# Performance work log

Hardware: AMD Instinct MI355X
Metric: run time of the kernel (lower is better)

## Reference

```python
import jax, jax.numpy as jnp
import numpy as np

B, T, C = 2, 2048, 2048
NH, G, HS = 16, 4, 128          # heads, kv groups, head dim
QPK = NH // G                    # queries per kv group
K = 4                            # conv kernel width
WIN = 512                        # sliding window (local_window)
SCALE = 1.0 / np.sqrt(HS)


def causal_conv1d_silu(x, w):
    # x: [B, T, D] channels-last, w: [D, K] depthwise kernel; causal left-pad then SiLU
    xp = jnp.pad(x, ((0, 0), (K - 1, 0), (0, 0)))
    out = sum(w[None, None, :, k] * xp[:, k:k + T, :] for k in range(K))
    return jax.nn.silu(out)


def apply_rope(x, cos, sin):
    # x: [B, T, H, HS], cos/sin: [T, HS//2]; non-interleaved halves rotation
    d = cos.shape[-1]
    x1, x2 = x[..., :d], x[..., d:]
    c = cos[None, :, None, :]
    s = sin[None, :, None, :]
    return jnp.concatenate([x1 * c - x2 * s, x1 * s + x2 * c], axis=-1)


def setup_inputs() -> dict:
    key = jax.random.key(0)
    ks = jax.random.split(key, 6)
    x = jax.random.normal(ks[0], (B, T, C), jnp.float32)
    Wqkv = jax.random.normal(ks[1], (C, (NH + 2 * G) * HS), jnp.float32) * 0.02
    Wproj = jax.random.normal(ks[2], (NH * HS, C), jnp.float32) * 0.02
    q_conv_w = jax.random.normal(ks[3], (NH * HS, K), jnp.float32) * 0.3
    k_conv_w = jax.random.normal(ks[4], (G * HS, K), jnp.float32) * 0.3
    v_conv_w = jax.random.normal(ks[5], (G * HS, K), jnp.float32) * 0.3
    # RoPE cache as in build_rope_cache
    theta = 1.0 / (10000.0 ** (jnp.arange(0, HS, 2, dtype=jnp.float32) / HS))
    idx = jnp.outer(jnp.arange(T, dtype=jnp.float32), theta)  # [T, HS//2]
    cos, sin = jnp.cos(idx), jnp.sin(idx)
    return {"x": x, "Wqkv": Wqkv, "Wproj": Wproj,
            "q_conv_w": q_conv_w, "k_conv_w": k_conv_w, "v_conv_w": v_conv_w,
            "cos": cos, "sin": sin}


def reference(x, Wqkv, Wproj, q_conv_w, k_conv_w, v_conv_w, cos, sin):
    # QKV projection + GQA split (group-major head layout, matches torch view/split)
    qkv = (x @ Wqkv).reshape(B, T, G, QPK + 2, HS)
    q = qkv[..., :QPK, :].reshape(B, T, NH * HS)
    k = qkv[..., QPK:QPK + 1, :].reshape(B, T, G * HS)
    v = qkv[..., QPK + 1:, :].reshape(B, T, G * HS)
    # short causal depthwise conv + silu on q/k/v
    q = causal_conv1d_silu(q, q_conv_w).reshape(B, T, NH, HS)
    k = causal_conv1d_silu(k, k_conv_w).reshape(B, T, G, HS)
    v = causal_conv1d_silu(v, v_conv_w).reshape(B, T, G, HS)
    # RoPE
    q = apply_rope(q, cos, sin)
    k = apply_rope(k, cos, sin)
    # expand kv groups to full heads (consecutive repeat matches group-major q)
    k = jnp.repeat(k, QPK, axis=2)  # [B, T, NH, HS]
    v = jnp.repeat(v, QPK, axis=2)
    # sliding-window causal attention
    scores = jnp.einsum('bthd,bshd->bhts', q, k) * SCALE  # [B, NH, T, T]
    i = jnp.arange(T)[:, None]
    j = jnp.arange(T)[None, :]
    mask = (j <= i) & (i - j < WIN)
    scores = jnp.where(mask, scores, jnp.finfo(scores.dtype).min)
    p = jax.nn.softmax(scores, axis=-1)
    y = jnp.einsum('bhts,bshd->bthd', p, v).reshape(B, T, NH * HS)
    return y @ Wproj
```

## Files before the change

### kernel.cpp

```cpp
#include <hip/hip_runtime.h>
#include <math.h>
#include <stdint.h>

#define B_    2
#define T_    2048
#define C_    2048
#define NH_   16
#define G_    4
#define HS_   128
#define WIN_  512
#define NQKV_ 3072
#define M_    4096
#define SCALE_ 0.08838834764831845f

typedef __attribute__((ext_vector_type(8))) __bf16 bf16x8;
typedef __attribute__((ext_vector_type(4))) float f32x4;
typedef unsigned short u16;

static __device__ __forceinline__ u16 f2bf(float f) {
  union { float f; unsigned u; } v; v.f = f;
  unsigned r = v.u + 0x7fffu + ((v.u >> 16) & 1u);
  return (u16)(r >> 16);
}
static __device__ __forceinline__ float bf2f(u16 h) {
  union { unsigned u; float f; } v; v.u = ((unsigned)h) << 16; return v.f;
}
static __device__ __forceinline__ bf16x8 ldg8(const u16* p) {
  return *(const bf16x8*)(const void*)p;
}

__global__ void prep_all(const float* __restrict__ x, const float* __restrict__ Wqkv,
                         const float* __restrict__ Wproj,
                         u16* __restrict__ x_bf, u16* __restrict__ wqkv_t,
                         u16* __restrict__ wproj_t) {
  int blk = blockIdx.x;
  if (blk < 8192) {
    int i = blk * 256 + threadIdx.x;
    float4 v = ((const float4*)x)[i];
    ushort4 o;
    o.x = f2bf(v.x); o.y = f2bf(v.y); o.z = f2bf(v.z); o.w = f2bf(v.w);
    ((ushort4*)x_bf)[i] = o;
    return;
  }
  __shared__ float tile[32][33];
  const float* in; u16* out; int R, Ccols, bx, by;
  if (blk < 8192 + 6144) {
    int idx = blk - 8192;
    in = Wqkv; out = wqkv_t; R = 2048; Ccols = 3072;
    bx = idx % 96; by = idx / 96;
  } else {
    int idx = blk - 14336;
    in = Wproj; out = wproj_t; R = 2048; Ccols = 2048;
    bx = idx & 63; by = idx >> 6;
  }
  int c0 = bx * 32, r0 = by * 32;
  int tx = threadIdx.x & 31, ty = threadIdx.x >> 5;
#pragma unroll
  for (int i = 0; i < 32; i += 8)
    tile[ty + i][tx] = in[(size_t)(r0 + ty + i) * Ccols + c0 + tx];
  __syncthreads();
#pragma unroll
  for (int i = 0; i < 32; i += 8)
    out[(size_t)(c0 + ty + i) * R + r0 + tx] = f2bf(tile[tx][ty + i]);
}

__global__ void transpose_v16(const u16* __restrict__ in, u16* __restrict__ out) {
  __shared__ u16 tile[32][33];
  int b = blockIdx.z;
  int c0 = blockIdx.x * 32, t0 = blockIdx.y * 32;
  int tx = threadIdx.x & 31, ty = threadIdx.x >> 5;
  const u16* src = in + (size_t)b * T_ * (G_*HS_);
  u16* dst = out + (size_t)b * (G_*HS_) * T_;
#pragma unroll
  for (int i = 0; i < 32; i += 8)
    tile[ty + i][tx] = src[(size_t)(t0 + ty + i) * (G_*HS_) + c0 + tx];
  __syncthreads();
#pragma unroll
  for (int i = 0; i < 32; i += 8)
    dst[(size_t)(c0 + ty + i) * T_ + t0 + tx] = tile[tx][ty + i];
}

template<int N, int K, int OUTBF>
__global__ __launch_bounds__(256)
void gemm_bt(const u16* __restrict__ A, const u16* __restrict__ Bt,
             u16* __restrict__ Cb, float* __restrict__ Cf) {
  __shared__ u16 lA[128 * 32];
  __shared__ u16 lB[128 * 32];
  const int m0 = blockIdx.x * 128;
  const int n0 = blockIdx.y * 128;
  const int lane = threadIdx.x & 63;
  const int wave = threadIdx.x >> 6;
  const int wr = (wave >> 1) * 64, wc = (wave & 1) * 64;
  const int fr = lane & 15, fk = (lane >> 4) * 8;
  const int srow = lane >> 2;
  const int scol = (lane & 3) * 8;
  f32x4 acc[4][4] = {};
  for (int k0 = 0; k0 < K; k0 += 32) {
#pragma unroll
    for (int c = 0; c < 2; ++c) {
      int chunk = wave * 2 + c;
      int row = chunk * 16 + srow;
      __builtin_amdgcn_global_load_lds(
          (__attribute__((address_space(1))) void*)(A + (size_t)(m0 + row) * K + k0 + scol),
          (__attribute__((address_space(3))) void*)(lA + chunk * 512), 16, 0, 0);
      __builtin_amdgcn_global_load_lds(
          (__attribute__((address_space(1))) void*)(Bt + (size_t)(n0 + row) * K + k0 + scol),
          (__attribute__((address_space(3))) void*)(lB + chunk * 512), 16, 0, 0);
    }
    __syncthreads();
    bf16x8 af[4], bb[4];
#pragma unroll
    for (int i = 0; i < 4; ++i) {
      af[i] = ldg8(lA + (wr + i * 16 + fr) * 32 + fk);
      bb[i] = ldg8(lB + (wc + i * 16 + fr) * 32 + fk);
    }
#pragma unroll
    for (int i = 0; i < 4; ++i)
#pragma unroll
      for (int j = 0; j < 4; ++j)
        acc[i][j] = __builtin_amdgcn_mfma_f32_16x16x32_bf16(af[i], bb[j], acc[i][j], 0, 0, 0);
    __syncthreads();
  }
  const int orow = m0 + wr + (lane >> 4) * 4;
  const int ocol = n0 + wc + fr;
#pragma unroll
  for (int i = 0; i < 4; ++i)
#pragma unroll
    for (int j = 0; j < 4; ++j)
#pragma unroll
      for (int jj = 0; jj < 4; ++jj) {
        int r = orow + i * 16 + jj, cc = ocol + j * 16;
        if (OUTBF) Cb[(size_t)r * N + cc] = f2bf(acc[i][j][jj]);
        else       Cf[(size_t)r * N + cc] = acc[i][j][jj];
      }
}

__global__ void conv_all(const u16* __restrict__ qkv, const float* __restrict__ qw,
                         const float* __restrict__ kw, const float* __restrict__ vw,
                         const float* __restrict__ cosT, const float* __restrict__ sinT,
                         u16* __restrict__ qout, u16* __restrict__ kout,
                         u16* __restrict__ vtmp) {
  int blk = blockIdx.x;
  const bf16x8 z8 = {};
  if (blk < 2048) {
    int tid = blk * 256 + threadIdx.x;
    int d8 = (tid & 7) << 3;
    int h  = (tid >> 3) & 15;
    int bt = tid >> 7;
    int t  = bt & (T_ - 1);
    int g = h >> 2, s = h & 3;
    int col = (g * 6 + s) * 128 + d8;
    const u16* p = qkv + (size_t)bt * NQKV_ + col;
    bf16x8 lo[4], hi[4];
#pragma unroll
    for (int k = 0; k < 4; ++k) {
      if (t + k >= 3) {
        long off = (long)(k - 3) * NQKV_;
        lo[k] = ldg8(p + off);
        hi[k] = ldg8(p + off + 64);
      } else { lo[k] = z8; hi[k] = z8; }
    }
    union { u16 a[8]; bf16x8 v; } olo, ohi;
#pragma unroll
    for (int j = 0; j < 8; ++j) {
      float4 wl = *(const float4*)(qw + (size_t)(h * 128 + d8 + j) * 4);
      float4 wh = *(const float4*)(qw + (size_t)(h * 128 + 64 + d8 + j) * 4);
      float a1 = wl.x * (float)lo[0][j] + wl.y * (float)lo[1][j] +
                 wl.z * (float)lo[2][j] + wl.w * (float)lo[3][j];
      float a2 = wh.x * (float)hi[0][j] + wh.y * (float)hi[1][j] +
                 wh.z * (float)hi[2][j] + wh.w * (float)hi[3][j];
      a1 = a1 / (1.f + __expf(-a1));
      a2 = a2 / (1.f + __expf(-a2));
      float c = cosT[t * 64 + d8 + j], sn = sinT[t * 64 + d8 + j];
      olo.a[j] = f2bf((a1 * c - a2 * sn) * SCALE_);
      ohi.a[j] = f2bf((a1 * sn + a2 * c) * SCALE_);
    }
    u16* dst = qout + ((size_t)bt * NH_ + h) * HS_ + d8;
    *(bf16x8*)(dst) = olo.v;
    *(bf16x8*)(dst + 64) = ohi.v;
  } else {
    int tid = (blk - 2048) * 256 + threadIdx.x;
    int idx = tid & 63;
    int bt  = tid >> 6;
    int t   = bt & (T_ - 1);
    int isv = idx >> 5;
    int g   = (idx >> 3) & 3;
    int d8  = (idx & 7) << 3;
    int col = (g * 6 + 4 + isv) * 128 + d8;
    const float* w = isv ? vw : kw;
    const u16* p = qkv + (size_t)bt * NQKV_ + col;
    bf16x8 lo[4], hi[4];
#pragma unroll
    for (int k = 0; k < 4; ++k) {
      if (t + k >= 3) {
        long off = (long)(k - 3) * NQKV_;
        lo[k] = ldg8(p + off);
        hi[k] = ldg8(p + off + 64);
      } else { lo[k] = z8; hi[k] = z8; }
    }
    float a1[8], a2[8];
#pragma unroll
    for (int j = 0; j < 8; ++j) {
      float4 wl = *(const float4*)(w + (size_t)(g * 128 + d8 + j) * 4);
      float4 wh = *(const float4*)(w + (size_t)(g * 128 + 64 + d8 + j) * 4);
      float x1 = wl.x * (float)lo[0][j] + wl.y * (float)lo[1][j] +
                 wl.z * (float)lo[2][j] + wl.w * (float)lo[3][j];
      float x2 = wh.x * (float)hi[0][j] + wh.y * (float)hi[1][j] +
                 wh.z * (float)hi[2][j] + wh.w * (float)hi[3][j];
      a1[j] = x1 / (1.f + __expf(-x1));
      a2[j] = x2 / (1.f + __expf(-x2));
    }
    union { u16 a[8]; bf16x8 v; } olo, ohi;
    if (isv == 0) {
#pragma unroll
      for (int j = 0; j < 8; ++j) {
        float c = cosT[t * 64 + d8 + j], sn = sinT[t * 64 + d8 + j];
        olo.a[j] = f2bf(a1[j] * c - a2[j] * sn);
        ohi.a[j] = f2bf(a1[j] * sn + a2[j] * c);
      }
      u16* dst = kout + ((size_t)bt * G_ + g) * HS_ + d8;
      *(bf16x8*)(dst) = olo.v;
      *(bf16x8*)(dst + 64) = ohi.v;
    } else {
#pragma unroll
      for (int j = 0; j < 8; ++j) {
        olo.a[j] = f2bf(a1[j]);
        ohi.a[j] = f2bf(a2[j]);
      }
      u16* dst = vtmp + ((size_t)bt * G_ + g) * HS_ + d8;
      *(bf16x8*)(dst) = olo.v;
      *(bf16x8*)(dst + 64) = ohi.v;
    }
  }
}

__global__ __launch_bounds__(256, 2)
void attn_swin(const u16* __restrict__ qbf, const u16* __restrict__ kbf,
               const u16* __restrict__ vt, u16* __restrict__ ybf) {
  __shared__ __align__(16) char kls[2][16384];
  __shared__ __align__(16) char vls[2][16384];
  __shared__ __align__(16) char pls[4][4096];
  const int lane = threadIdx.x & 63;
  const int wave = threadIdx.x >> 6;
  const int btile = blockIdx.x & 15;
  const int h  = (blockIdx.x >> 4) & 15;
  const int b  = blockIdx.x >> 8;
  const int g  = h >> 2;
  const int t0b = btile << 7;
  const int t0w = t0b + wave * 32;
  const int fr = lane & 15;
  const int hi = lane >> 4;
  const int fko = hi * 8;
  char* pl = pls[wave];
  const int swz = (fr & 7) << 4;

  const int krow_l = (lane >> 4);
  const int kcb    = (lane & 15) * 16;
  const int vrow_l = (lane >> 3);
  const int vcb    = (lane & 7) * 16;

  bf16x8 qf[2][4];
#pragma unroll
  for (int qh = 0; qh < 2; ++qh) {
    const u16* qb = qbf + ((size_t)((b * T_ + t0w + qh * 16 + fr) * NH_ + h)) * HS_ + fko;
#pragma unroll
    for (int kc = 0; kc < 4; ++kc) qf[qh][kc] = ldg8(qb + kc * 32);
  }

  int sbeg = t0b - (WIN_ - 1); if (sbeg < 0) sbeg = 0; sbeg &= ~63;
  const int nt = (t0b + 128 - sbeg) >> 6;

  const char* kgbase = (const char*)kbf + (((size_t)(b * T_) * G_ + g) * HS_) * 2;
  const char* vgbase = (const char*)vt + ((size_t)(b * (G_*HS_) + g * HS_)) * T_ * 2;

  auto stage = [&](int bufi, int s0) {
    char* kb = kls[bufi]; char* vb = vls[bufi];
#pragma unroll
    for (int c = 0; c < 4; ++c) {
      int i = wave * 4 + c;
      {
        int row = i * 4 + krow_l;
        int scb = kcb ^ ((row & 7) << 4);
        const char* src = kgbase + (size_t)(s0 + row) * (G_*HS_*2) + scb;
        __builtin_amdgcn_global_load_lds(
            (__attribute__((address_space(1))) void*)src,
            (__attribute__((address_space(3))) void*)(kb + i * 1024), 16, 0, 0);
      }
      {
        int row = i * 8 + vrow_l;
        int scb = vcb ^ ((row & 7) << 4);
        const char* src = vgbase + (size_t)row * (T_*2) + (size_t)s0 * 2 + scb;
        __builtin_amdgcn_global_load_lds(
            (__attribute__((address_space(1))) void*)src,
            (__attribute__((address_space(3))) void*)(vb + i * 1024), 16, 0, 0);
      }
    }
  };

  f32x4 acc_o[2][8];
#pragma unroll
  for (int qh = 0; qh < 2; ++qh)
#pragma unroll
    for (int n = 0; n < 8; ++n) acc_o[qh][n] = (f32x4){0.f, 0.f, 0.f, 0.f};
  float m_r[2] = {-1e30f, -1e30f}, l_r[2] = {0.f, 0.f};

  stage(0, sbeg);
  __syncthreads();
  int cur = 0;

  for (int t = 0; t < nt; ++t) {
    int s0 = sbeg + (t << 6);
    if (t + 1 < nt) stage(cur ^ 1, s0 + 64);
    const char* kb = kls[cur];
    const char* vb = vls[cur];

    f32x4 st[2][4];
#pragma unroll
    for (int qh = 0; qh < 2; ++qh)
#pragma unroll
      for (int c = 0; c < 4; ++c) st[qh][c] = (f32x4){0.f, 0.f, 0.f, 0.f};
    __builtin_amdgcn_s_setprio(1);
#pragma unroll
    for (int c = 0; c < 4; ++c) {
      int row = c * 16 + fr;
#pragma unroll
      for (int kc = 0; kc < 4; ++kc) {
        bf16x8 kf = *(const bf16x8*)(kb + row * 256 + ((kc * 64 + hi * 16) ^ swz));
        st[0][c] = __builtin_amdgcn_mfma_f32_16x16x32_bf16(kf, qf[0][kc], st[0][c], 0, 0, 0);
        st[1][c] = __builtin_amdgcn_mfma_f32_16x16x32_bf16(kf, qf[1][kc], st[1][c], 0, 0, 0);
      }
    }
    __builtin_amdgcn_s_setprio(0);

#pragma unroll
    for (int qh = 0; qh < 2; ++qh) {
      int qr = t0w + qh * 16 + fr;
      float tmax = -1e30f;
#pragma unroll
      for (int c = 0; c < 4; ++c)
#pragma unroll
        for (int j = 0; j < 4; ++j) {
          int key = s0 + c * 16 + hi * 4 + j;
          int dlt = qr - key;
          float x = (dlt >= 0 && dlt < WIN_) ? st[qh][c][j] : -1e30f;
          st[qh][c][j] = x;
          tmax = fmaxf(tmax, x);
        }
      tmax = fmaxf(tmax, __shfl_xor(tmax, 16, 64));
      tmax = fmaxf(tmax, __shfl_xor(tmax, 32, 64));
      float fac = 1.f;
      bool need = !__all(tmax <= m_r[qh] + 8.f);
      if (need) {
        float mn = fmaxf(m_r[qh], tmax);
        fac = __expf(m_r[qh] - mn);
        m_r[qh] = mn;
      }
      float ps = 0.f;
#pragma unroll
      for (int c = 0; c < 4; ++c) {
        union { ushort4 u4; __bf16 hh[4]; } pk;
#pragma unroll
        for (int j = 0; j < 4; ++j) {
          float p = (st[qh][c][j] > -1e29f) ? __expf(st[qh][c][j] - m_r[qh]) : 0.f;
          ps += p;
          pk.hh[j] = (__bf16)p;
        }
        *(ushort4*)(pl + (qh * 16 + fr) * 128 + ((c * 32 + hi * 8) ^ swz)) = pk.u4;
      }
      ps += __shfl_xor(ps, 16, 64);
      ps += __shfl_xor(ps, 32, 64);
      l_r[qh] = l_r[qh] * fac + ps;
      if (need) {
        float fq0 = __shfl(fac, hi * 4 + 0, 64);
        float fq1 = __shfl(fac, hi * 4 + 1, 64);
        float fq2 = __shfl(fac, hi * 4 + 2, 64);
        float fq3 = __shfl(fac, hi * 4 + 3, 64);
#pragma unroll
        for (int n = 0; n < 8; ++n) {
          acc_o[qh][n][0] *= fq0; acc_o[qh][n][1] *= fq1;
          acc_o[qh][n][2] *= fq2; acc_o[qh][n][3] *= fq3;
        }
      }
    }

#pragma unroll
    for (int ch = 0; ch < 2; ++ch) {
      bf16x8 pa0 = *(const bf16x8*)(pl + fr * 128 + ((ch * 64 + hi * 16) ^ swz));
      bf16x8 pa1 = *(const bf16x8*)(pl + (16 + fr) * 128 + ((ch * 64 + hi * 16) ^ swz));
      __builtin_amdgcn_s_setprio(1);
#pragma unroll
      for (int n = 0; n < 8; ++n) {
        int row = n * 16 + fr;
        bf16x8 vf = *(const bf16x8*)(vb + row * 128 + ((ch * 64 + hi * 16) ^ swz));
        acc_o[0][n] = __builtin_amdgcn_mfma_f32_16x16x32_bf16(pa0, vf, acc_o[0][n], 0, 0, 0);
        acc_o[1][n] = __builtin_amdgcn_mfma_f32_16x16x32_bf16(pa1, vf, acc_o[1][n], 0, 0, 0);
      }
      __builtin_amdgcn_s_setprio(0);
    }
    __syncthreads();
    cur ^= 1;
  }

#pragma unroll
  for (int qh = 0; qh < 2; ++qh) {
    float inv = 1.f / l_r[qh];
    float iq[4];
#pragma unroll
    for (int j = 0; j < 4; ++j) iq[j] = __shfl(inv, hi * 4 + j, 64);
#pragma unroll
    for (int n = 0; n < 8; ++n)
#pragma unroll
      for (int jj = 0; jj < 4; ++jj) {
        int t = t0w + qh * 16 + hi * 4 + jj;
        ybf[((size_t)(b * T_ + t)) * (NH_*HS_) + h * HS_ + n * 16 + fr] =
            f2bf(acc_o[qh][n][jj] * iq[jj]);
      }
  }
}

extern "C" void kernel_launch(void* const* d_in, const int* in_sizes, int n_in,
                              void* d_out, int out_size, void* d_ws, size_t ws_size,
                              hipStream_t stream) {
  (void)in_sizes; (void)n_in; (void)out_size;
  const float* x     = (const float*)d_in[0];
  const float* Wqkv  = (const float*)d_in[1];
  const float* Wproj = (const float*)d_in[2];
  const float* qw    = (const float*)d_in[3];
  const float* kw    = (const float*)d_in[4];
  const float* vw    = (const float*)d_in[5];
  const float* cosT  = (const float*)d_in[6];
  const float* sinT  = (const float*)d_in[7];
  float* out = (float*)d_out;
  char* ws = (char*)d_ws;

  u16* x_bf    = (u16*)(ws + 0);
  u16* wqkv_t  = (u16*)(ws + 16777216);
  u16* wproj_t = (u16*)(ws + 29360128);
  u16* qkv_bf  = (u16*)(ws + 37748736);
  u16* q_bf    = (u16*)(ws + 62914560);
  u16* k_bf    = (u16*)(ws + 79691776);
  u16* v_tmp   = (u16*)(ws + 83886080);
  u16* v_t     = (u16*)(ws + 88080384);
  u16* y_bf    = (u16*)(ws + 92274688);
  if (ws_size < (size_t)109051904) return;

  prep_all<<<18432, 256, 0, stream>>>(x, Wqkv, Wproj, x_bf, wqkv_t, wproj_t);
  gemm_bt<3072, 2048, 1><<<dim3(32, 24), 256, 0, stream>>>(x_bf, wqkv_t, qkv_bf, nullptr);
  conv_all<<<3072, 256, 0, stream>>>(qkv_bf, qw, kw, vw, cosT, sinT, q_bf, k_bf, v_tmp);
  transpose_v16<<<dim3(16, 64, 2), 256, 0, stream>>>(v_tmp, v_t);
  attn_swin<<<512, 256, 0, stream>>>(q_bf, k_bf, v_t, y_bf);
  gemm_bt<2048, 2048, 0><<<dim3(32, 16), 256, 0, stream>>>(y_bf, wproj_t, nullptr, out);
}
```

Before: 204.2 us.

## Halve attention query tile, load V fragments directly from global, skip inactive tiles

The attention kernel now processes 64 query rows per block (16 per wave) instead of 128, doubling the grid to 1024 blocks and raising launch bounds to 4 blocks per CU. V is no longer staged through LDS; each wave loads its V fragments straight from global memory into registers, which cuts LDS use. Waves also skip key tiles that fall entirely outside their own window. The aim is more occupancy and less wasted masked work, at the cost of less K/V reuse per block and more global traffic for V.

```diff
diff --git a/kernel.cpp b/kernel.cpp
--- a/kernel.cpp
+++ b/kernel.cpp
@@ -234,75 +234,60 @@
   }
 }
 
-__global__ __launch_bounds__(256, 2)
+__global__ __launch_bounds__(256, 4)
 void attn_swin(const u16* __restrict__ qbf, const u16* __restrict__ kbf,
                const u16* __restrict__ vt, u16* __restrict__ ybf) {
   __shared__ __align__(16) char kls[2][16384];
-  __shared__ __align__(16) char vls[2][16384];
-  __shared__ __align__(16) char pls[4][4096];
+  __shared__ __align__(16) char pls[4][2048];
   const int lane = threadIdx.x & 63;
   const int wave = threadIdx.x >> 6;
-  const int btile = blockIdx.x & 15;
-  const int h  = (blockIdx.x >> 4) & 15;
-  const int b  = blockIdx.x >> 8;
+  const int btile = blockIdx.x & 31;
+  const int h  = (blockIdx.x >> 5) & 15;
+  const int b  = blockIdx.x >> 9;
   const int g  = h >> 2;
-  const int t0b = btile << 7;
-  const int t0w = t0b + wave * 32;
+  const int t0b = btile << 6;
+  const int t0w = t0b + wave * 16;
   const int fr = lane & 15;
   const int hi = lane >> 4;
   const int fko = hi * 8;
+  const int qr = t0w + fr;
   char* pl = pls[wave];
   const int swz = (fr & 7) << 4;
 
   const int krow_l = (lane >> 4);
   const int kcb    = (lane & 15) * 16;
-  const int vrow_l = (lane >> 3);
-  const int vcb    = (lane & 7) * 16;
-
-  bf16x8 qf[2][4];
-#pragma unroll
-  for (int qh = 0; qh < 2; ++qh) {
-    const u16* qb = qbf + ((size_t)((b * T_ + t0w + qh * 16 + fr) * NH_ + h)) * HS_ + fko;
-#pragma unroll
-    for (int kc = 0; kc < 4; ++kc) qf[qh][kc] = ldg8(qb + kc * 32);
+
+  bf16x8 qf[4];
+  {
+    const u16* qb = qbf + ((size_t)((b * T_ + t0w + fr) * NH_ + h)) * HS_ + fko;
+#pragma unroll
+    for (int kc = 0; kc < 4; ++kc) qf[kc] = ldg8(qb + kc * 32);
   }
 
   int sbeg = t0b - (WIN_ - 1); if (sbeg < 0) sbeg = 0; sbeg &= ~63;
-  const int nt = (t0b + 128 - sbeg) >> 6;
+  const int nt = (t0b + 64 - sbeg) >> 6;
 
   const char* kgbase = (const char*)kbf + (((size_t)(b * T_) * G_ + g) * HS_) * 2;
-  const char* vgbase = (const char*)vt + ((size_t)(b * (G_*HS_) + g * HS_)) * T_ * 2;
+  const u16* vrow = vt + (size_t)(b * (G_*HS_) + g * HS_ + fr) * T_ + fko;
 
   auto stage = [&](int bufi, int s0) {
-    char* kb = kls[bufi]; char* vb = vls[bufi];
+    char* kb = kls[bufi];
 #pragma unroll
     for (int c = 0; c < 4; ++c) {
       int i = wave * 4 + c;
-      {
-        int row = i * 4 + krow_l;
-        int scb = kcb ^ ((row & 7) << 4);
-        const char* src = kgbase + (size_t)(s0 + row) * (G_*HS_*2) + scb;
-        __builtin_amdgcn_global_load_lds(
-            (__attribute__((address_space(1))) void*)src,
-            (__attribute__((address_space(3))) void*)(kb + i * 1024), 16, 0, 0);
-      }
-      {
-        int row = i * 8 + vrow_l;
-        int scb = vcb ^ ((row & 7) << 4);
-        const char* src = vgbase + (size_t)row * (T_*2) + (size_t)s0 * 2 + scb;
-        __builtin_amdgcn_global_load_lds(
-            (__attribute__((address_space(1))) void*)src,
-            (__attribute__((address_space(3))) void*)(vb + i * 1024), 16, 0, 0);
-      }
+      int row = i * 4 + krow_l;
+      int scb = kcb ^ ((row & 7) << 4);
+      const char* src = kgbase + (size_t)(s0 + row) * (G_*HS_*2) + scb;
+      __builtin_amdgcn_global_load_lds(
+          (__attribute__((address_space(1))) void*)src,
+          (__attribute__((address_space(3))) void*)(kb + i * 1024), 16, 0, 0);
     }
   };
 
-  f32x4 acc_o[2][8];
-#pragma unroll
-  for (int qh = 0; qh < 2; ++qh)
-#pragma unroll
-    for (int n = 0; n < 8; ++n) acc_o[qh][n] = (f32x4){0.f, 0.f, 0.f, 0.f};
-  float m_r[2] = {-1e30f, -1e30f}, l_r[2] = {0.f, 0.f};
+  f32x4 acc_o[8];
+#pragma unroll
+  for (int n = 0; n < 8; ++n) acc_o[n] = (f32x4){0.f, 0.f, 0.f, 0.f};
+  float m_r = -1e30f, l_r = 0.f;
 
   stage(0, sbeg);
   __syncthreads();
@@ -311,30 +296,32 @@
   for (int t = 0; t < nt; ++t) {
     int s0 = sbeg + (t << 6);
     if (t + 1 < nt) stage(cur ^ 1, s0 + 64);
-    const char* kb = kls[cur];
-    const char* vb = vls[cur];
-
-    f32x4 st[2][4];
-#pragma unroll
-    for (int qh = 0; qh < 2; ++qh)
-#pragma unroll
-      for (int c = 0; c < 4; ++c) st[qh][c] = (f32x4){0.f, 0.f, 0.f, 0.f};
-    __builtin_amdgcn_s_setprio(1);
-#pragma unroll
-    for (int c = 0; c < 4; ++c) {
-      int row = c * 16 + fr;
-#pragma unroll
-      for (int kc = 0; kc < 4; ++kc) {
-        bf16x8 kf = *(const bf16x8*)(kb + row * 256 + ((kc * 64 + hi * 16) ^ swz));
-        st[0][c] = __builtin_amdgcn_mfma_f32_16x16x32_bf16(kf, qf[0][kc], st[0][c], 0, 0, 0);
-        st[1][c] = __builtin_amdgcn_mfma_f32_16x16x32_bf16(kf, qf[1][kc], st[1][c], 0, 0, 0);
-      }
-    }
-    __builtin_amdgcn_s_setprio(0);
-
-#pragma unroll
-    for (int qh = 0; qh < 2; ++qh) {
-      int qr = t0w + qh * 16 + fr;
+    bool active = (s0 <= t0w + 15) && (s0 + 63 >= t0w - (WIN_ - 1));
+    if (active) {
+      const char* kb = kls[cur];
+
+      bf16x8 vf0[8];
+#pragma unroll
+      for (int n = 0; n < 8; ++n) vf0[n] = ldg8(vrow + (size_t)(n * 16) * T_ + s0);
+
+      f32x4 st[4];
+      __builtin_amdgcn_s_setprio(1);
+#pragma unroll
+      for (int c = 0; c < 4; ++c) {
+        st[c] = (f32x4){0.f, 0.f, 0.f, 0.f};
+        int row = c * 16 + fr;
+#pragma unroll
+        for (int kc = 0; kc < 4; ++kc) {
+          bf16x8 kf = *(const bf16x8*)(kb + row * 256 + ((kc * 64 + hi * 16) ^ swz));
+          st[c] = __builtin_amdgcn_mfma_f32_16x16x32_bf16(kf, qf[kc], st[c], 0, 0, 0);
+        }
+      }
+      __builtin_amdgcn_s_setprio(0);
+
+      bf16x8 vf1[8];
+#pragma unroll
+      for (int n = 0; n < 8; ++n) vf1[n] = ldg8(vrow + (size_t)(n * 16) * T_ + s0 + 32);
+
       float tmax = -1e30f;
 #pragma unroll
       for (int c = 0; c < 4; ++c)
@@ -342,34 +329,36 @@
         for (int j = 0; j < 4; ++j) {
           int key = s0 + c * 16 + hi * 4 + j;
           int dlt = qr - key;
-          float x = (dlt >= 0 && dlt < WIN_) ? st[qh][c][j] : -1e30f;
-          st[qh][c][j] = x;
+          float x = (dlt >= 0 && dlt < WIN_) ? st[c][j] : -1e30f;
+          st[c][j] = x;
           tmax = fmaxf(tmax, x);
         }
       tmax = fmaxf(tmax, __shfl_xor(tmax, 16, 64));
       tmax = fmaxf(tmax, __shfl_xor(tmax, 32, 64));
       float fac = 1.f;
-      bool need = !__all(tmax <= m_r[qh] + 8.f);
+      bool need = !__all(tmax <= m_r + 8.f);
       if (need) {
-        float mn = fmaxf(m_r[qh], tmax);
-        fac = __expf(m_r[qh] - mn);
-        m_r[qh] = mn;
-      }
+        float mn = fmaxf(m_r, tmax);
+        fac = __expf(m_r - mn);
+        m_r = mn;
+      }
+
       float ps = 0.f;
 #pragma unroll
       for (int c = 0; c < 4; ++c) {
         union { ushort4 u4; __bf16 hh[4]; } pk;
 #pragma unroll
         for (int j = 0; j < 4; ++j) {
-          float p = (st[qh][c][j] > -1e29f) ? __expf(st[qh][c][j] - m_r[qh]) : 0.f;
+          float p = (st[c][j] > -1e29f) ? __expf(st[c][j] - m_r) : 0.f;
           ps += p;
           pk.hh[j] = (__bf16)p;
         }
-        *(ushort4*)(pl + (qh * 16 + fr) * 128 + ((c * 32 + hi * 8) ^ swz)) = pk.u4;
+        *(ushort4*)(pl + fr * 128 + ((c * 32 + hi * 8) ^ swz)) = pk.u4;
       }
       ps += __shfl_xor(ps, 16, 64);
       ps += __shfl_xor(ps, 32, 64);
-      l_r[qh] = l_r[qh] * fac + ps;
+      l_r = l_r * fac + ps;
+
       if (need) {
         float fq0 = __shfl(fac, hi * 4 + 0, 64);
         float fq1 = __shfl(fac, hi * 4 + 1, 64);
@@ -377,45 +366,39 @@
         float fq3 = __shfl(fac, hi * 4 + 3, 64);
 #pragma unroll
         for (int n = 0; n < 8; ++n) {
-          acc_o[qh][n][0] *= fq0; acc_o[qh][n][1] *= fq1;
-          acc_o[qh][n][2] *= fq2; acc_o[qh][n][3] *= fq3;
+          acc_o[n][0] *= fq0; acc_o[n][1] *= fq1;
+          acc_o[n][2] *= fq2; acc_o[n][3] *= fq3;
         }
       }
-    }
-
-#pragma unroll
-    for (int ch = 0; ch < 2; ++ch) {
-      bf16x8 pa0 = *(const bf16x8*)(pl + fr * 128 + ((ch * 64 + hi * 16) ^ swz));
-      bf16x8 pa1 = *(const bf16x8*)(pl + (16 + fr) * 128 + ((ch * 64 + hi * 16) ^ swz));
-      __builtin_amdgcn_s_setprio(1);
-#pragma unroll
-      for (int n = 0; n < 8; ++n) {
-        int row = n * 16 + fr;
-        bf16x8 vf = *(const bf16x8*)(vb + row * 128 + ((ch * 64 + hi * 16) ^ swz));
-        acc_o[0][n] = __builtin_amdgcn_mfma_f32_16x16x32_bf16(pa0, vf, acc_o[0][n], 0, 0, 0);
-        acc_o[1][n] = __builtin_amdgcn_mfma_f32_16x16x32_bf16(pa1, vf, acc_o[1][n], 0, 0, 0);
-      }
-      __builtin_amdgcn_s_setprio(0);
+
+      {
+        bf16x8 pa0 = *(const bf16x8*)(pl + fr * 128 + ((0 * 64 + hi * 16) ^ swz));
+        bf16x8 pa1 = *(const bf16x8*)(pl + fr * 128 + ((1 * 64 + hi * 16) ^ swz));
+        __builtin_amdgcn_s_setprio(1);
+#pragma unroll
+        for (int n = 0; n < 8; ++n)
+          acc_o[n] = __builtin_amdgcn_mfma_f32_16x16x32_bf16(pa0, vf0[n], acc_o[n], 0, 0, 0);
+#pragma unroll
+        for (int n = 0; n < 8; ++n)
+          acc_o[n] = __builtin_amdgcn_mfma_f32_16x16x32_bf16(pa1, vf1[n], acc_o[n], 0, 0, 0);
+        __builtin_amdgcn_s_setprio(0);
+      }
     }
     __syncthreads();
     cur ^= 1;
   }
 
-#pragma unroll
-  for (int qh = 0; qh < 2; ++qh) {
-    float inv = 1.f / l_r[qh];
-    float iq[4];
-#pragma unroll
-    for (int j = 0; j < 4; ++j) iq[j] = __shfl(inv, hi * 4 + j, 64);
-#pragma unroll
-    for (int n = 0; n < 8; ++n)
-#pragma unroll
-      for (int jj = 0; jj < 4; ++jj) {
-        int t = t0w + qh * 16 + hi * 4 + jj;
-        ybf[((size_t)(b * T_ + t)) * (NH_*HS_) + h * HS_ + n * 16 + fr] =
-            f2bf(acc_o[qh][n][jj] * iq[jj]);
-      }
-  }
+  float inv = 1.f / l_r;
+  float iq[4];
+#pragma unroll
+  for (int j = 0; j < 4; ++j) iq[j] = __shfl(inv, hi * 4 + j, 64);
+#pragma unroll
+  for (int n = 0; n < 8; ++n)
+#pragma unroll
+    for (int jj = 0; jj < 4; ++jj) {
+      int t = t0w + hi * 4 + jj;
+      ybf[((size_t)(b * T_ + t)) * (NH_*HS_) + h * HS_ + n * 16 + fr] = f2bf(acc_o[n][jj] * iq[jj]);
+    }
 }
 
 extern "C" void kernel_launch(void* const* d_in, const int* in_sizes, int n_in,
@@ -448,6 +431,6 @@
   gemm_bt<3072, 2048, 1><<<dim3(32, 24), 256, 0, stream>>>(x_bf, wqkv_t, qkv_bf, nullptr);
   conv_all<<<3072, 256, 0, stream>>>(qkv_bf, qw, kw, vw, cosT, sinT, q_bf, k_bf, v_tmp);
   transpose_v16<<<dim3(16, 64, 2), 256, 0, stream>>>(v_tmp, v_t);
-  attn_swin<<<512, 256, 0, stream>>>(q_bf, k_bf, v_t, y_bf);
+  attn_swin<<<1024, 256, 0, stream>>>(q_bf, k_bf, v_t, y_bf);
   gemm_bt<2048, 2048, 0><<<dim3(32, 16), 256, 0, stream>>>(y_bf, wproj_t, nullptr, out);
 }
```

Result: slower. 302.8 us (+48.3%).
